# Performance work log

Measured on AMD Instinct MI355X. Metric: run time of the kernel, lower is better.

The kernel has to match this reference:

```python
import jax, jax.numpy as jnp
import numpy as np

N_NODES = 100000
N_EDGES = 1600000
D_IN = 128
D_H = 128
N_LAYERS = 3
N_OUT = 10
N_GRAPHS = 64


def setup_inputs() -> dict:
    key = jax.random.key(0)
    ks = jax.random.split(key, 12)
    glorot = lambda k, fi, fo: jax.random.normal(k, (fi, fo), jnp.float32) * np.sqrt(2.0 / (fi + fo))
    return {
        "x": jax.random.normal(ks[0], (N_NODES, D_IN), jnp.float32),
        "edge_index": jax.random.randint(ks[1], (2, N_EDGES), 0, N_NODES, jnp.int64 if jax.config.jax_enable_x64 else jnp.int32),
        "batch": jnp.sort(jax.random.randint(ks[2], (N_NODES,), 0, N_GRAPHS)),
        "target_size": N_GRAPHS,
        "W1": glorot(ks[3], D_IN, D_H), "b1": jnp.zeros((D_H,), jnp.float32),
        "W2": glorot(ks[4], D_H, D_H), "b2": jnp.zeros((D_H,), jnp.float32),
        "W3": glorot(ks[5], D_H, D_H), "b3": jnp.zeros((D_H,), jnp.float32),
        "lin1_w": glorot(ks[6], N_LAYERS * D_H, D_H), "lin1_b": jnp.zeros((D_H,), jnp.float32),
        "lin2_w": glorot(ks[7], D_H, N_OUT), "lin2_b": jnp.zeros((N_OUT,), jnp.float32),
    }


def _gcn_conv(x, src, dst, norm, W, b, n_nodes):
    # PyG GCNConv: h = X W; out[dst] += norm * h[src]; out += b
    h = x @ W
    msg = h[src] * norm[:, None]            # [E+N, D_H] gathered messages
    out = jax.ops.segment_sum(msg, dst, num_segments=n_nodes)
    return out + b


def reference(x, edge_index, batch, target_size, W1, b1, W2, b2, W3, b3,
              lin1_w, lin1_b, lin2_w, lin2_b):
    n = x.shape[0]
    loops = jnp.arange(n, dtype=edge_index.dtype)
    src = jnp.concatenate([edge_index[0], loops])   # add self-loops (PyG default)
    dst = jnp.concatenate([edge_index[1], loops])
    deg = jax.ops.segment_sum(jnp.ones_like(src, dtype=x.dtype), dst, num_segments=n)
    dinv = jnp.where(deg > 0, jax.lax.rsqrt(deg), 0.0)
    norm = dinv[src] * dinv[dst]                    # symmetric normalization

    h1 = jax.nn.relu(_gcn_conv(x, src, dst, norm, W1, b1, n))
    h2 = jax.nn.relu(_gcn_conv(h1, src, dst, norm, W2, b2, n))
    h3 = jax.nn.relu(_gcn_conv(h2, src, dst, norm, W3, b3, n))
    h = jnp.concatenate([h1, h2, h3], axis=-1)      # JumpingKnowledge 'cat' -> [N, 3*D_H]

    # global_mean_pool over graphs
    counts = jax.ops.segment_sum(jnp.ones((n,), x.dtype), batch, num_segments=target_size)
    pooled = jax.ops.segment_sum(h, batch, num_segments=target_size)
    pooled = pooled / jnp.maximum(counts, 1.0)[:, None]

    g = jax.nn.relu(pooled @ lin1_w + lin1_b)       # dropout is identity at inference
    logits = g @ lin2_w + lin2_b
    return jax.nn.log_softmax(logits, axis=-1)
```

## Files before the change

### kernel.cpp

```cpp
#include <hip/hip_runtime.h>

#define NN 100000
#define NE 1600000
#define DH 128
#define NG 64

#define NBUCKU 98
#define EPB 4096
#define NBLK_BIN 391
#define CAP 20480

#define LDH 136

typedef __attribute__((ext_vector_type(2))) _Float16 half2v;
typedef __attribute__((ext_vector_type(4))) _Float16 half4;
typedef __attribute__((ext_vector_type(8))) _Float16 half8;
typedef __attribute__((ext_vector_type(4))) float f32x4;

__device__ inline unsigned int enc8(_Float16 h) {
  unsigned short b = __builtin_bit_cast(unsigned short, h);
  unsigned short r = (unsigned short)(b + 0x7F + ((b >> 8) & 1));
  return (unsigned int)(r >> 8);
}
__device__ inline half2v d02(unsigned int u) {
  return __builtin_bit_cast(half2v, (u << 8) & 0xFF00FF00u);
}
__device__ inline half2v d13(unsigned int u) {
  return __builtin_bit_cast(half2v, u & 0xFF00FF00u);
}


__global__ __launch_bounds__(256) void k_build(const int* __restrict__ esrc,
                                               const int* __restrict__ edst,
                                               const int* __restrict__ batch,
                                               const float* __restrict__ W0,
                                               const float* __restrict__ W1,
                                               const float* __restrict__ W2,
                                               int* __restrict__ bucketCursor,
                                               unsigned int* __restrict__ pairs,
                                               int* __restrict__ startg,
                                               _Float16* __restrict__ Wt) {
  int b = blockIdx.x, t = threadIdx.x;
  int gtid = b * 256 + t;

  if (gtid < 3 * DH * DH) {
    int l = gtid >> 14;
    int rem = gtid & 16383;
    int n = rem >> 7, k = rem & 127;
    const float* W = (l == 0) ? W0 : (l == 1) ? W1 : W2;
    Wt[(size_t)l * DH * DH + n * DH + k] = (_Float16)W[k * DH + n];
  }
  if (gtid < NN) {
    int bat = batch[gtid];
    int prev = (gtid == 0) ? -1 : batch[gtid - 1];
    for (int g = prev + 1; g <= bat; ++g) startg[g] = gtid;
    if (gtid == NN - 1)
      for (int g = bat + 1; g <= NG; ++g) startg[g] = NN;
  }

  __shared__ int h[NBUCKU];
  __shared__ int cur[NBUCKU];
  if (t < NBUCKU) h[t] = 0;
  __syncthreads();
  int base = b * EPB;
#pragma unroll
  for (int i = 0; i < EPB / 256; ++i) {
    int e = base + i * 256 + t;
    if (e < NE) atomicAdd(&h[edst[e] >> 10], 1);
  }
  __syncthreads();
  if (t < NBUCKU) {
    int rel = atomicAdd(&bucketCursor[t], h[t]);
    cur[t] = t * CAP + rel;
  }
  __syncthreads();
#pragma unroll
  for (int i = 0; i < EPB / 256; ++i) {
    int e = base + i * 256 + t;
    if (e < NE) {
      int d = edst[e];
      int q = atomicAdd(&cur[d >> 10], 1);
      pairs[q] = ((unsigned int)esrc[e] << 10) | (unsigned int)(d & 1023);
    }
  }
}


__global__ __launch_bounds__(256) void k_finalize(const unsigned int* __restrict__ pairs,
                                                  const int* __restrict__ bucketCursor,
                                                  int* __restrict__ offA,
                                                  int* __restrict__ offB,
                                                  float* __restrict__ dinv,
                                                  int* __restrict__ csr_src) {
  __shared__ int cnt[1024];
  __shared__ int tsum[256];
  int b = blockIdx.x, t = threadIdx.x;
  int nodeBase = b << 10;
  for (int i = t; i < 1024; i += 256) cnt[i] = 0;
  __syncthreads();
  int pStart = b * CAP;
  int pEnd = pStart + bucketCursor[b];
  for (int p = pStart + t; p < pEnd; p += 256)
    atomicAdd(&cnt[pairs[p] & 1023], 1);
  __syncthreads();
  int c0 = cnt[t * 4], c1 = cnt[t * 4 + 1], c2 = cnt[t * 4 + 2], c3 = cnt[t * 4 + 3];
  tsum[t] = c0 + c1 + c2 + c3;
  __syncthreads();
  for (int off = 1; off < 256; off <<= 1) {
    int v = (t >= off) ? tsum[t - off] : 0;
    __syncthreads();
    tsum[t] += v;
    __syncthreads();
  }
  int basep = pStart + ((t > 0) ? tsum[t - 1] : 0);
  int e0 = basep, e1 = basep + c0, e2 = e1 + c1, e3 = e2 + c2;
  __syncthreads();
  cnt[t * 4] = e0; cnt[t * 4 + 1] = e1; cnt[t * 4 + 2] = e2; cnt[t * 4 + 3] = e3;
  int g = nodeBase + t * 4;
  if (g < NN)     { offA[g] = e0;     offB[g] = e1;      dinv[g] = rsqrtf((float)c0 + 1.f); }
  if (g + 1 < NN) { offA[g + 1] = e1; offB[g + 1] = e2;  dinv[g + 1] = rsqrtf((float)c1 + 1.f); }
  if (g + 2 < NN) { offA[g + 2] = e2; offB[g + 2] = e3;  dinv[g + 2] = rsqrtf((float)c2 + 1.f); }
  if (g + 3 < NN) { offA[g + 3] = e3; offB[g + 3] = e3 + c3; dinv[g + 3] = rsqrtf((float)c3 + 1.f); }
  __syncthreads();
  for (int p = pStart + t; p < pEnd; p += 256) {
    unsigned int pr = pairs[p];
    int pos = atomicAdd(&cnt[pr & 1023], 1);
    csr_src[pos] = (int)(pr >> 10);
  }
}


template <bool F32IN>
__global__ __launch_bounds__(256) void k_gemm(const void* __restrict__ Ap,
                                              const _Float16* __restrict__ Wt,
                                              const float* __restrict__ dinv,
                                              unsigned char* __restrict__ Out8) {
  __shared__ _Float16 Wl[128 * LDH];
  int tid = threadIdx.x;
  int rowBase = blockIdx.x * 128;

#pragma unroll
  for (int i = 0; i < 8; ++i) {
    int chunk = tid + i * 256;
    int r = chunk >> 4, c = (chunk & 15) * 8;
    *(half8*)&Wl[r * LDH + c] = *(const half8*)(Wt + r * DH + c);
  }

  int wv = tid >> 6;
  int lane = tid & 63;
  int n16 = lane & 15;
  int quad = lane >> 4;

  int r0 = rowBase + wv * 32 + n16;
  int r1 = r0 + 16;

  half8 af[2][4];
  if (F32IN) {
    const float* A = (const float*)Ap;
#pragma unroll
    for (int kk = 0; kk < 4; ++kk) {
      half8 z = {};
      if (r0 < NN) {
        float4 lo = *(const float4*)(A + (size_t)r0 * DH + quad * 8 + kk * 32);
        float4 hi = *(const float4*)(A + (size_t)r0 * DH + quad * 8 + kk * 32 + 4);
        z = (half8){(_Float16)lo.x, (_Float16)lo.y, (_Float16)lo.z, (_Float16)lo.w,
                    (_Float16)hi.x, (_Float16)hi.y, (_Float16)hi.z, (_Float16)hi.w};
      }
      af[0][kk] = z;
      half8 z1 = {};
      if (r1 < NN) {
        float4 lo = *(const float4*)(A + (size_t)r1 * DH + quad * 8 + kk * 32);
        float4 hi = *(const float4*)(A + (size_t)r1 * DH + quad * 8 + kk * 32 + 4);
        z1 = (half8){(_Float16)lo.x, (_Float16)lo.y, (_Float16)lo.z, (_Float16)lo.w,
                     (_Float16)hi.x, (_Float16)hi.y, (_Float16)hi.z, (_Float16)hi.w};
      }
      af[1][kk] = z1;
    }
  } else {
    const _Float16* A = (const _Float16*)Ap;
#pragma unroll
    for (int kk = 0; kk < 4; ++kk) {
      half8 z = {};
      if (r0 < NN) z = *(const half8*)(A + (size_t)r0 * DH + quad * 8 + kk * 32);
      af[0][kk] = z;
      half8 z1 = {};
      if (r1 < NN) z1 = *(const half8*)(A + (size_t)r1 * DH + quad * 8 + kk * 32);
      af[1][kk] = z1;
    }
  }
  __syncthreads();

  f32x4 acc[2][8];
#pragma unroll
  for (int mt = 0; mt < 2; ++mt)
#pragma unroll
    for (int ct = 0; ct < 8; ++ct) acc[mt][ct] = (f32x4){0.f, 0.f, 0.f, 0.f};

  const _Float16* bp = &Wl[n16 * LDH + quad * 8];
#pragma unroll
  for (int kk = 0; kk < 4; ++kk) {
#pragma unroll
    for (int ct = 0; ct < 8; ++ct) {
      half8 bf = *(const half8*)(bp + (size_t)ct * 16 * LDH + kk * 32);
      acc[0][ct] = __builtin_amdgcn_mfma_f32_16x16x32_f16(af[0][kk], bf, acc[0][ct], 0, 0, 0);
      acc[1][ct] = __builtin_amdgcn_mfma_f32_16x16x32_f16(af[1][kk], bf, acc[1][ct], 0, 0, 0);
    }
  }

  float dv[2][4];
#pragma unroll
  for (int mt = 0; mt < 2; ++mt)
#pragma unroll
    for (int r = 0; r < 4; ++r) {
      int gr = rowBase + wv * 32 + mt * 16 + quad * 4 + r;
      dv[mt][r] = (gr < NN) ? dinv[gr] : 0.f;
    }

  __syncthreads();
#pragma unroll
  for (int mt = 0; mt < 2; ++mt)
#pragma unroll
    for (int ct = 0; ct < 8; ++ct)
#pragma unroll
      for (int r = 0; r < 4; ++r)
        Wl[(wv * 32 + mt * 16 + quad * 4 + r) * LDH + ct * 16 + n16] =
            (_Float16)(acc[mt][ct][r] * dv[mt][r]);
  __syncthreads();

#pragma unroll
  for (int i = 0; i < 8; ++i) {
    int chunk = tid + i * 256;
    int r = chunk >> 4, c = (chunk & 15) * 8;
    int gr = rowBase + r;
    if (gr < NN) {
      half8 v = *(const half8*)&Wl[r * LDH + c];
      unsigned int lo = enc8(v[0]) | (enc8(v[1]) << 8) | (enc8(v[2]) << 16) | (enc8(v[3]) << 24);
      unsigned int hi = enc8(v[4]) | (enc8(v[5]) << 8) | (enc8(v[6]) << 16) | (enc8(v[7]) << 24);
      uint2 st = {lo, hi};
      *(uint2*)(Out8 + (size_t)gr * DH + c) = st;
    }
  }
}


__global__ __launch_bounds__(512) void k_fused(const unsigned char* __restrict__ hs8_in,
                                               const int* __restrict__ csr_src,
                                               const int* __restrict__ offA,
                                               const int* __restrict__ offB,
                                               const float* __restrict__ dinv,
                                               const float* __restrict__ bias,
                                               const int* __restrict__ batch,
                                               const int* __restrict__ startg,
                                               float* __restrict__ pooled,
                                               int colOff,
                                               const _Float16* __restrict__ Wt,
                                               unsigned char* __restrict__ hs8_out) {
  __shared__ _Float16 Hl[64 * LDH];
  __shared__ _Float16 Wl[128 * LDH];
  int tid = threadIdx.x;
  int n0 = blockIdx.x * 64;

#pragma unroll
  for (int i = 0; i < 4; ++i) {
    int chunk = tid + i * 512;
    int r = chunk >> 4, c = (chunk & 15) * 8;
    *(half8*)&Wl[r * LDH + c] = *(const half8*)(Wt + r * DH + c);
  }

  int nd = tid >> 3;
  int part = tid & 7;
  int n = n0 + nd;
  bool valid = (n < NN);

  half2v acc[8];
#pragma unroll
  for (int i = 0; i < 8; ++i) acc[i] = (half2v){(_Float16)0, (_Float16)0};

  if (valid) {
    const unsigned char* bp = hs8_in + part * 16;
    uint4 us = *(const uint4*)(bp + (size_t)n * DH);
    acc[0] += d02(us.x); acc[1] += d13(us.x);
    acc[2] += d02(us.y); acc[3] += d13(us.y);
    acc[4] += d02(us.z); acc[5] += d13(us.z);
    acc[6] += d02(us.w); acc[7] += d13(us.w);
    int s = offA[n], e = offB[n];
    int p = s;
    for (; p + 3 < e; p += 4) {
      int s0 = csr_src[p], s1 = csr_src[p + 1], s2 = csr_src[p + 2], s3 = csr_src[p + 3];
      uint4 u0 = *(const uint4*)(bp + (size_t)s0 * DH);
      uint4 u1 = *(const uint4*)(bp + (size_t)s1 * DH);
      uint4 u2 = *(const uint4*)(bp + (size_t)s2 * DH);
      uint4 u3 = *(const uint4*)(bp + (size_t)s3 * DH);
      acc[0] += d02(u0.x); acc[1] += d13(u0.x); acc[2] += d02(u0.y); acc[3] += d13(u0.y);
      acc[4] += d02(u0.z); acc[5] += d13(u0.z); acc[6] += d02(u0.w); acc[7] += d13(u0.w);
      acc[0] += d02(u1.x); acc[1] += d13(u1.x); acc[2] += d02(u1.y); acc[3] += d13(u1.y);
      acc[4] += d02(u1.z); acc[5] += d13(u1.z); acc[6] += d02(u1.w); acc[7] += d13(u1.w);
      acc[0] += d02(u2.x); acc[1] += d13(u2.x); acc[2] += d02(u2.y); acc[3] += d13(u2.y);
      acc[4] += d02(u2.z); acc[5] += d13(u2.z); acc[6] += d02(u2.w); acc[7] += d13(u2.w);
      acc[0] += d02(u3.x); acc[1] += d13(u3.x); acc[2] += d02(u3.y); acc[3] += d13(u3.y);
      acc[4] += d02(u3.z); acc[5] += d13(u3.z); acc[6] += d02(u3.w); acc[7] += d13(u3.w);
    }
    for (; p < e; ++p) {
      int s0 = csr_src[p];
      uint4 u0 = *(const uint4*)(bp + (size_t)s0 * DH);
      acc[0] += d02(u0.x); acc[1] += d13(u0.x); acc[2] += d02(u0.y); acc[3] += d13(u0.y);
      acc[4] += d02(u0.z); acc[5] += d13(u0.z); acc[6] += d02(u0.w); acc[7] += d13(u0.w);
    }
  }

  float dv = valid ? dinv[n] : 0.f;
#pragma unroll
  for (int w = 0; w < 4; ++w) {
    int dim = part * 16 + w * 4;
    float4 b4 = *(const float4*)(bias + dim);
    float h0 = valid ? fmaxf(fmaf((float)acc[2 * w][0], dv, b4.x), 0.f) : 0.f;
    float h1 = valid ? fmaxf(fmaf((float)acc[2 * w + 1][0], dv, b4.y), 0.f) : 0.f;
    float h2 = valid ? fmaxf(fmaf((float)acc[2 * w][1], dv, b4.z), 0.f) : 0.f;
    float h3 = valid ? fmaxf(fmaf((float)acc[2 * w + 1][1], dv, b4.w), 0.f) : 0.f;
    half4 hh = {(_Float16)h0, (_Float16)h1, (_Float16)h2, (_Float16)h3};
    *(half4*)&Hl[nd * LDH + dim] = hh;
  }
  __syncthreads();

  if (tid < DH) {
    int nEnd = (n0 + 64 < NN) ? n0 + 64 : NN;
    int gF = batch[n0];
    int gL = batch[nEnd - 1];
    for (int g = gF; g <= gL; ++g) {
      int rs = (startg[g] > n0) ? startg[g] : n0;
      int re = (startg[g + 1] < nEnd) ? startg[g + 1] : nEnd;
      if (re > rs) {
        float sum = 0.f;
        for (int r2 = rs; r2 < re; ++r2) sum += (float)Hl[(r2 - n0) * LDH + tid];
        atomicAdd(&pooled[g * (3 * DH) + colOff + tid], sum);
      }
    }
  }

  int wv = tid >> 6;
  int lane = tid & 63;
  int n16 = lane & 15;
  int quad = lane >> 4;
  int m16 = wv >> 1;
  int ctB = (wv & 1) * 4;

  f32x4 acc2[4];
#pragma unroll
  for (int ct = 0; ct < 4; ++ct) acc2[ct] = (f32x4){0.f, 0.f, 0.f, 0.f};

  const _Float16* ap = &Hl[(m16 * 16 + n16) * LDH + quad * 8];
#pragma unroll
  for (int kk = 0; kk < 4; ++kk) {
    half8 af = *(const half8*)(ap + kk * 32);
#pragma unroll
    for (int ct = 0; ct < 4; ++ct) {
      half8 bf = *(const half8*)&Wl[((ctB + ct) * 16 + n16) * LDH + quad * 8 + kk * 32];
      acc2[ct] = __builtin_amdgcn_mfma_f32_16x16x32_f16(af, bf, acc2[ct], 0, 0, 0);
    }
  }

  float dvo[4];
#pragma unroll
  for (int rr = 0; rr < 4; ++rr) {
    int gr = n0 + m16 * 16 + quad * 4 + rr;
    dvo[rr] = (gr < NN) ? dinv[gr] : 0.f;
  }

  __syncthreads();
#pragma unroll
  for (int ct = 0; ct < 4; ++ct)
#pragma unroll
    for (int rr = 0; rr < 4; ++rr)
      Hl[(m16 * 16 + quad * 4 + rr) * LDH + (ctB + ct) * 16 + n16] =
          (_Float16)(acc2[ct][rr] * dvo[rr]);
  __syncthreads();

#pragma unroll
  for (int i = 0; i < 2; ++i) {
    int chunk = tid + i * 512;
    int r = chunk >> 4, c = (chunk & 15) * 8;
    int gr = n0 + r;
    if (gr < NN) {
      half8 v = *(const half8*)&Hl[r * LDH + c];
      unsigned int lo = enc8(v[0]) | (enc8(v[1]) << 8) | (enc8(v[2]) << 16) | (enc8(v[3]) << 24);
      unsigned int hi = enc8(v[4]) | (enc8(v[5]) << 8) | (enc8(v[6]) << 16) | (enc8(v[7]) << 24);
      uint2 st = {lo, hi};
      *(uint2*)(hs8_out + (size_t)gr * DH + c) = st;
    }
  }
}


__global__ __launch_bounds__(256) void k_aggregate(const unsigned char* __restrict__ hs8,
                                                   const int* __restrict__ csr_src,
                                                   const int* __restrict__ offA,
                                                   const int* __restrict__ offB,
                                                   const float* __restrict__ dinv,
                                                   const float* __restrict__ bias,
                                                   const int* __restrict__ batch,
                                                   float* __restrict__ pooled,
                                                   int colOff) {
  __shared__ float stage[8][DH];
  int tid = threadIdx.x;
  int gid = blockIdx.x * 256 + tid;
  int node = gid >> 5;
  int sub = tid >> 5;
  int lane4 = (gid & 31) * 4;
  int s = offA[node];
  int e = offB[node];

  unsigned int us = *(const unsigned int*)(hs8 + (size_t)node * DH + lane4);
  half2v aE0 = d02(us), aE1 = d13(us);
  half2v aO0 = {(_Float16)0, (_Float16)0}, aO1 = {(_Float16)0, (_Float16)0};

  int p = s;
  for (; p + 3 < e; p += 4) {
    int s0 = csr_src[p];
    int s1 = csr_src[p + 1];
    int s2 = csr_src[p + 2];
    int s3 = csr_src[p + 3];
    unsigned int u0 = *(const unsigned int*)(hs8 + (size_t)s0 * DH + lane4);
    unsigned int u1 = *(const unsigned int*)(hs8 + (size_t)s1 * DH + lane4);
    unsigned int u2 = *(const unsigned int*)(hs8 + (size_t)s2 * DH + lane4);
    unsigned int u3 = *(const unsigned int*)(hs8 + (size_t)s3 * DH + lane4);
    aE0 += d02(u0); aE1 += d13(u0);
    aO0 += d02(u1); aO1 += d13(u1);
    aE0 += d02(u2); aE1 += d13(u2);
    aO0 += d02(u3); aO1 += d13(u3);
  }
  for (; p < e; ++p) {
    int s0 = csr_src[p];
    unsigned int u0 = *(const unsigned int*)(hs8 + (size_t)s0 * DH + lane4);
    aE0 += d02(u0); aE1 += d13(u0);
  }

  float ax = (float)aE0[0] + (float)aO0[0];
  float ay = (float)aE1[0] + (float)aO1[0];
  float az = (float)aE0[1] + (float)aO0[1];
  float aw = (float)aE1[1] + (float)aO1[1];

  float dv = dinv[node];
  float4 b4 = *(const float4*)(bias + lane4);
  float4 r;
  r.x = fmaxf(fmaf(ax, dv, b4.x), 0.f);
  r.y = fmaxf(fmaf(ay, dv, b4.y), 0.f);
  r.z = fmaxf(fmaf(az, dv, b4.z), 0.f);
  r.w = fmaxf(fmaf(aw, dv, b4.w), 0.f);

  int nodeFirst = blockIdx.x * 8;
  int gFirst = batch[nodeFirst];
  int gLast = batch[nodeFirst + 7];
  if (gFirst == gLast) {
    *(float4*)&stage[sub][lane4] = r;
    __syncthreads();
    if (tid < DH) {
      float ssum = 0.f;
#pragma unroll
      for (int w = 0; w < 8; ++w) ssum += stage[w][tid];
      atomicAdd(&pooled[gFirst * (3 * DH) + colOff + tid], ssum);
    }
  } else {
    int g = batch[node];
    float* pp = &pooled[g * (3 * DH) + colOff + lane4];
    atomicAdd(pp + 0, r.x);
    atomicAdd(pp + 1, r.y);
    atomicAdd(pp + 2, r.z);
    atomicAdd(pp + 3, r.w);
  }
}


__global__ __launch_bounds__(128) void k_head(const float* __restrict__ pooled,
                                              const int* __restrict__ startg,
                                              const float* __restrict__ l1w,
                                              const float* __restrict__ l1b,
                                              const float* __restrict__ l2w,
                                              const float* __restrict__ l2b,
                                              float* __restrict__ out) {
  __shared__ float pr[3 * DH];
  __shared__ float grow[DH];
  __shared__ float lg[16];
  int g = blockIdx.x, t = threadIdx.x;
  float cnt = (float)(startg[g + 1] - startg[g]);
  float inv = 1.0f / fmaxf(cnt, 1.0f);
  for (int k = t; k < 3 * DH; k += 128) pr[k] = pooled[g * (3 * DH) + k] * inv;
  __syncthreads();
  float acc = l1b[t];
  for (int k = 0; k < 3 * DH; ++k) acc = fmaf(pr[k], l1w[k * DH + t], acc);
  grow[t] = fmaxf(acc, 0.f);
  __syncthreads();
  if (t < 10) {
    float a = l2b[t];
    for (int k = 0; k < DH; ++k) a = fmaf(grow[k], l2w[k * 10 + t], a);
    lg[t] = a;
  }
  __syncthreads();
  if (t < 10) {
    float m = lg[0];
    for (int i = 1; i < 10; ++i) m = fmaxf(m, lg[i]);
    float sum = 0.f;
    for (int i = 0; i < 10; ++i) sum += expf(lg[i] - m);
    out[g * 10 + t] = lg[t] - m - logf(sum);
  }
}


extern "C" void kernel_launch(void* const* d_in, const int* in_sizes, int n_in,
                              void* d_out, int out_size, void* d_ws, size_t ws_size,
                              hipStream_t stream) {
  const float* x = (const float*)d_in[0];
  const int* ei = (const int*)d_in[1];
  const int* esrc = ei;
  const int* edst = ei + NE;
  const int* batch = (const int*)d_in[2];
  const float* W0 = (const float*)d_in[4];
  const float* W1 = (const float*)d_in[6];
  const float* W2 = (const float*)d_in[8];
  const float* B[3] = {(const float*)d_in[5], (const float*)d_in[7], (const float*)d_in[9]};
  const float* l1w = (const float*)d_in[10];
  const float* l1b = (const float*)d_in[11];
  const float* l2w = (const float*)d_in[12];
  const float* l2b = (const float*)d_in[13];
  float* out = (float*)d_out;

  char* ws = (char*)d_ws;
  size_t off = 0;
  auto alloc = [&](size_t bytes) {
    char* p = ws + off;
    off = (off + bytes + 255) & ~(size_t)255;
    return p;
  };
  float* pooled = (float*)alloc((size_t)NG * 3 * DH * 4);
  int* bucketCursor = (int*)alloc(NBUCKU * 4);
  size_t msBytes = (size_t)NG * 3 * DH * 4 + 512;

  int* offA = (int*)alloc((size_t)NN * 4);
  int* offB = (int*)alloc((size_t)NN * 4);
  float* dinv = (float*)alloc((size_t)NN * 4);
  int* startg = (int*)alloc((NG + 1) * 4);
  _Float16* Wt = (_Float16*)alloc((size_t)3 * DH * DH * 2);
  unsigned char* hs8A = (unsigned char*)alloc((size_t)NN * DH);
  unsigned char* hs8B = (unsigned char*)alloc((size_t)NN * DH);
  unsigned int* pairs = (unsigned int*)alloc((size_t)NBUCKU * CAP * 4);
  int* csr_src = (int*)alloc((size_t)NBUCKU * CAP * 4);

  hipMemsetAsync(pooled, 0, msBytes, stream);

  k_build<<<NBLK_BIN, 256, 0, stream>>>(esrc, edst, batch, W0, W1, W2,
                                        bucketCursor, pairs, startg, Wt);
  k_finalize<<<NBUCKU, 256, 0, stream>>>(pairs, bucketCursor, offA, offB, dinv, csr_src);

  k_gemm<true><<<(NN + 127) / 128, 256, 0, stream>>>((const void*)x, Wt, dinv, hs8A);

  int nFusedBlk = (NN + 63) / 64;
  k_fused<<<nFusedBlk, 512, 0, stream>>>(hs8A, csr_src, offA, offB, dinv, B[0], batch,
                                         startg, pooled, 0,
                                         Wt + (size_t)1 * DH * DH, hs8B);
  k_fused<<<nFusedBlk, 512, 0, stream>>>(hs8B, csr_src, offA, offB, dinv, B[1], batch,
                                         startg, pooled, DH,
                                         Wt + (size_t)2 * DH * DH, hs8A);

  k_aggregate<<<(NN * 32) / 256, 256, 0, stream>>>(hs8A, csr_src, offA, offB, dinv, B[2],
                                                   batch, pooled, 2 * DH);

  k_head<<<NG, 128, 0, stream>>>(pooled, startg, l1w, l1b, l2w, l2b, out);
}
```

Measured before the change: 365.9 us.

## Restructure final aggregation to 8 threads per node with 16-byte gathers and block pooling

The last-layer aggregation kernel now assigns 8 threads per node, with each thread loading 16 bytes (16 fp8 features) per neighbor instead of 32 threads loading 4 bytes each. A block handles 64 nodes and uses an 8-way unrolled gather loop. Pooling is done per block by summing staged rows over graph ranges taken from startg, so each block issues per-graph atomics instead of falling back to per-element atomics when a block spans two graphs. Wider loads reduce the number of memory instructions per edge. In exchange, each thread holds more registers and parallelism per node is lower.

```diff
diff --git a/kernel.cpp b/kernel.cpp
--- a/kernel.cpp
+++ b/kernel.cpp
@@ -11,6 +11,7 @@
 #define CAP 20480
 
 #define LDH 136
+#define LDF 132
 
 typedef __attribute__((ext_vector_type(2))) _Float16 half2v;
 typedef __attribute__((ext_vector_type(4))) _Float16 half4;
@@ -391,81 +392,115 @@
 }
 
 
-__global__ __launch_bounds__(256) void k_aggregate(const unsigned char* __restrict__ hs8,
+__global__ __launch_bounds__(512) void k_aggregate(const unsigned char* __restrict__ hs8,
                                                    const int* __restrict__ csr_src,
                                                    const int* __restrict__ offA,
                                                    const int* __restrict__ offB,
                                                    const float* __restrict__ dinv,
                                                    const float* __restrict__ bias,
                                                    const int* __restrict__ batch,
+                                                   const int* __restrict__ startg,
                                                    float* __restrict__ pooled,
                                                    int colOff) {
-  __shared__ float stage[8][DH];
+  __shared__ float stage[64][LDF];
   int tid = threadIdx.x;
-  int gid = blockIdx.x * 256 + tid;
-  int node = gid >> 5;
-  int sub = tid >> 5;
-  int lane4 = (gid & 31) * 4;
-  int s = offA[node];
-  int e = offB[node];
-
-  unsigned int us = *(const unsigned int*)(hs8 + (size_t)node * DH + lane4);
-  half2v aE0 = d02(us), aE1 = d13(us);
-  half2v aO0 = {(_Float16)0, (_Float16)0}, aO1 = {(_Float16)0, (_Float16)0};
-
-  int p = s;
-  for (; p + 3 < e; p += 4) {
-    int s0 = csr_src[p];
-    int s1 = csr_src[p + 1];
-    int s2 = csr_src[p + 2];
-    int s3 = csr_src[p + 3];
-    unsigned int u0 = *(const unsigned int*)(hs8 + (size_t)s0 * DH + lane4);
-    unsigned int u1 = *(const unsigned int*)(hs8 + (size_t)s1 * DH + lane4);
-    unsigned int u2 = *(const unsigned int*)(hs8 + (size_t)s2 * DH + lane4);
-    unsigned int u3 = *(const unsigned int*)(hs8 + (size_t)s3 * DH + lane4);
-    aE0 += d02(u0); aE1 += d13(u0);
-    aO0 += d02(u1); aO1 += d13(u1);
-    aE0 += d02(u2); aE1 += d13(u2);
-    aO0 += d02(u3); aO1 += d13(u3);
-  }
-  for (; p < e; ++p) {
-    int s0 = csr_src[p];
-    unsigned int u0 = *(const unsigned int*)(hs8 + (size_t)s0 * DH + lane4);
-    aE0 += d02(u0); aE1 += d13(u0);
-  }
-
-  float ax = (float)aE0[0] + (float)aO0[0];
-  float ay = (float)aE1[0] + (float)aO1[0];
-  float az = (float)aE0[1] + (float)aO0[1];
-  float aw = (float)aE1[1] + (float)aO1[1];
-
-  float dv = dinv[node];
-  float4 b4 = *(const float4*)(bias + lane4);
-  float4 r;
-  r.x = fmaxf(fmaf(ax, dv, b4.x), 0.f);
-  r.y = fmaxf(fmaf(ay, dv, b4.y), 0.f);
-  r.z = fmaxf(fmaf(az, dv, b4.z), 0.f);
-  r.w = fmaxf(fmaf(aw, dv, b4.w), 0.f);
-
-  int nodeFirst = blockIdx.x * 8;
-  int gFirst = batch[nodeFirst];
-  int gLast = batch[nodeFirst + 7];
-  if (gFirst == gLast) {
-    *(float4*)&stage[sub][lane4] = r;
-    __syncthreads();
-    if (tid < DH) {
-      float ssum = 0.f;
-#pragma unroll
-      for (int w = 0; w < 8; ++w) ssum += stage[w][tid];
-      atomicAdd(&pooled[gFirst * (3 * DH) + colOff + tid], ssum);
-    }
-  } else {
-    int g = batch[node];
-    float* pp = &pooled[g * (3 * DH) + colOff + lane4];
-    atomicAdd(pp + 0, r.x);
-    atomicAdd(pp + 1, r.y);
-    atomicAdd(pp + 2, r.z);
-    atomicAdd(pp + 3, r.w);
+  int n0 = blockIdx.x * 64;
+  int nd = tid >> 3;
+  int part = tid & 7;
+  int n = n0 + nd;
+  bool valid = (n < NN);
+
+  half2v acc[8];
+#pragma unroll
+  for (int i = 0; i < 8; ++i) acc[i] = (half2v){(_Float16)0, (_Float16)0};
+
+  if (valid) {
+    const unsigned char* bp = hs8 + part * 16;
+    uint4 us = *(const uint4*)(bp + (size_t)n * DH);
+    acc[0] += d02(us.x); acc[1] += d13(us.x);
+    acc[2] += d02(us.y); acc[3] += d13(us.y);
+    acc[4] += d02(us.z); acc[5] += d13(us.z);
+    acc[6] += d02(us.w); acc[7] += d13(us.w);
+    int s = offA[n], e = offB[n];
+    int p = s;
+    for (; p + 7 < e; p += 8) {
+      int s0 = csr_src[p],     s1 = csr_src[p + 1], s2 = csr_src[p + 2], s3 = csr_src[p + 3];
+      int s4 = csr_src[p + 4], s5 = csr_src[p + 5], s6 = csr_src[p + 6], s7 = csr_src[p + 7];
+      uint4 u0 = *(const uint4*)(bp + (size_t)s0 * DH);
+      uint4 u1 = *(const uint4*)(bp + (size_t)s1 * DH);
+      uint4 u2 = *(const uint4*)(bp + (size_t)s2 * DH);
+      uint4 u3 = *(const uint4*)(bp + (size_t)s3 * DH);
+      uint4 u4 = *(const uint4*)(bp + (size_t)s4 * DH);
+      uint4 u5 = *(const uint4*)(bp + (size_t)s5 * DH);
+      uint4 u6 = *(const uint4*)(bp + (size_t)s6 * DH);
+      uint4 u7 = *(const uint4*)(bp + (size_t)s7 * DH);
+      acc[0] += d02(u0.x); acc[1] += d13(u0.x); acc[2] += d02(u0.y); acc[3] += d13(u0.y);
+      acc[4] += d02(u0.z); acc[5] += d13(u0.z); acc[6] += d02(u0.w); acc[7] += d13(u0.w);
+      acc[0] += d02(u1.x); acc[1] += d13(u1.x); acc[2] += d02(u1.y); acc[3] += d13(u1.y);
+      acc[4] += d02(u1.z); acc[5] += d13(u1.z); acc[6] += d02(u1.w); acc[7] += d13(u1.w);
+      acc[0] += d02(u2.x); acc[1] += d13(u2.x); acc[2] += d02(u2.y); acc[3] += d13(u2.y);
+      acc[4] += d02(u2.z); acc[5] += d13(u2.z); acc[6] += d02(u2.w); acc[7] += d13(u2.w);
+      acc[0] += d02(u3.x); acc[1] += d13(u3.x); acc[2] += d02(u3.y); acc[3] += d13(u3.y);
+      acc[4] += d02(u3.z); acc[5] += d13(u3.z); acc[6] += d02(u3.w); acc[7] += d13(u3.w);
+      acc[0] += d02(u4.x); acc[1] += d13(u4.x); acc[2] += d02(u4.y); acc[3] += d13(u4.y);
+      acc[4] += d02(u4.z); acc[5] += d13(u4.z); acc[6] += d02(u4.w); acc[7] += d13(u4.w);
+      acc[0] += d02(u5.x); acc[1] += d13(u5.x); acc[2] += d02(u5.y); acc[3] += d13(u5.y);
+      acc[4] += d02(u5.z); acc[5] += d13(u5.z); acc[6] += d02(u5.w); acc[7] += d13(u5.w);
+      acc[0] += d02(u6.x); acc[1] += d13(u6.x); acc[2] += d02(u6.y); acc[3] += d13(u6.y);
+      acc[4] += d02(u6.z); acc[5] += d13(u6.z); acc[6] += d02(u6.w); acc[7] += d13(u6.w);
+      acc[0] += d02(u7.x); acc[1] += d13(u7.x); acc[2] += d02(u7.y); acc[3] += d13(u7.y);
+      acc[4] += d02(u7.z); acc[5] += d13(u7.z); acc[6] += d02(u7.w); acc[7] += d13(u7.w);
+    }
+    for (; p + 3 < e; p += 4) {
+      int s0 = csr_src[p], s1 = csr_src[p + 1], s2 = csr_src[p + 2], s3 = csr_src[p + 3];
+      uint4 u0 = *(const uint4*)(bp + (size_t)s0 * DH);
+      uint4 u1 = *(const uint4*)(bp + (size_t)s1 * DH);
+      uint4 u2 = *(const uint4*)(bp + (size_t)s2 * DH);
+      uint4 u3 = *(const uint4*)(bp + (size_t)s3 * DH);
+      acc[0] += d02(u0.x); acc[1] += d13(u0.x); acc[2] += d02(u0.y); acc[3] += d13(u0.y);
+      acc[4] += d02(u0.z); acc[5] += d13(u0.z); acc[6] += d02(u0.w); acc[7] += d13(u0.w);
+      acc[0] += d02(u1.x); acc[1] += d13(u1.x); acc[2] += d02(u1.y); acc[3] += d13(u1.y);
+      acc[4] += d02(u1.z); acc[5] += d13(u1.z); acc[6] += d02(u1.w); acc[7] += d13(u1.w);
+      acc[0] += d02(u2.x); acc[1] += d13(u2.x); acc[2] += d02(u2.y); acc[3] += d13(u2.y);
+      acc[4] += d02(u2.z); acc[5] += d13(u2.z); acc[6] += d02(u2.w); acc[7] += d13(u2.w);
+      acc[0] += d02(u3.x); acc[1] += d13(u3.x); acc[2] += d02(u3.y); acc[3] += d13(u3.y);
+      acc[4] += d02(u3.z); acc[5] += d13(u3.z); acc[6] += d02(u3.w); acc[7] += d13(u3.w);
+    }
+    for (; p < e; ++p) {
+      int s0 = csr_src[p];
+      uint4 u0 = *(const uint4*)(bp + (size_t)s0 * DH);
+      acc[0] += d02(u0.x); acc[1] += d13(u0.x); acc[2] += d02(u0.y); acc[3] += d13(u0.y);
+      acc[4] += d02(u0.z); acc[5] += d13(u0.z); acc[6] += d02(u0.w); acc[7] += d13(u0.w);
+    }
+  }
+
+  float dv = valid ? dinv[n] : 0.f;
+#pragma unroll
+  for (int w = 0; w < 4; ++w) {
+    int dim = part * 16 + w * 4;
+    float4 b4 = *(const float4*)(bias + dim);
+    float4 r;
+    r.x = valid ? fmaxf(fmaf((float)acc[2 * w][0], dv, b4.x), 0.f) : 0.f;
+    r.y = valid ? fmaxf(fmaf((float)acc[2 * w + 1][0], dv, b4.y), 0.f) : 0.f;
+    r.z = valid ? fmaxf(fmaf((float)acc[2 * w][1], dv, b4.z), 0.f) : 0.f;
+    r.w = valid ? fmaxf(fmaf((float)acc[2 * w + 1][1], dv, b4.w), 0.f) : 0.f;
+    *(float4*)&stage[nd][dim] = r;
+  }
+  __syncthreads();
+
+  if (tid < DH) {
+    int nEnd = (n0 + 64 < NN) ? n0 + 64 : NN;
+    int gF = batch[n0];
+    int gL = batch[nEnd - 1];
+    for (int g = gF; g <= gL; ++g) {
+      int rs = (startg[g] > n0) ? startg[g] : n0;
+      int re = (startg[g + 1] < nEnd) ? startg[g + 1] : nEnd;
+      if (re > rs) {
+        float sum = 0.f;
+        for (int r2 = rs; r2 < re; ++r2) sum += stage[r2 - n0][tid];
+        atomicAdd(&pooled[g * (3 * DH) + colOff + tid], sum);
+      }
+    }
   }
 }
 
@@ -560,8 +595,8 @@
                                          startg, pooled, DH,
                                          Wt + (size_t)2 * DH * DH, hs8A);
 
-  k_aggregate<<<(NN * 32) / 256, 256, 0, stream>>>(hs8A, csr_src, offA, offB, dinv, B[2],
-                                                   batch, pooled, 2 * DH);
+  k_aggregate<<<nFusedBlk, 512, 0, stream>>>(hs8A, csr_src, offA, offB, dinv, B[2],
+                                             batch, startg, pooled, 2 * DH);
 
   k_head<<<NG, 128, 0, stream>>>(pooled, startg, l1w, l1b, l2w, l2b, out);
 }
```

Result: faster. 349.8 us (-4.4%).
